# Kernel optimization log

Measured on AMD Instinct MI355X. Metric: run time of the kernel, lower is better.

The kernel has to match this reference:

```python
import jax, jax.numpy as jnp
import numpy as np

B, L, D, H = 2, 2048, 1024, 16
HD = D // H


def setup_inputs() -> dict:
    key = jax.random.key(0)
    ks = jax.random.split(key, 12)
    s = 1.0 / np.sqrt(D)
    inp = {
        "q": jax.random.normal(ks[0], (B, L, D), jnp.float32),
        "k": jax.random.normal(ks[1], (B, L, D), jnp.float32),
        "v": jax.random.normal(ks[2], (B, L, D), jnp.float32),
        "mask": jnp.zeros((B, L), dtype=bool),  # True = masked out
        "Wq": jax.random.normal(ks[3], (D, D), jnp.float32) * s,
        "bq": jnp.zeros((D,), jnp.float32),
        "Wk": jax.random.normal(ks[4], (D, D), jnp.float32) * s,
        "bk": jnp.zeros((D,), jnp.float32),
        "Wv": jax.random.normal(ks[5], (D, D), jnp.float32) * s,
        "bv": jnp.zeros((D,), jnp.float32),
        "Wo": jax.random.normal(ks[6], (D, D), jnp.float32) * s,
        "bo": jnp.zeros((D,), jnp.float32),
    }
    return inp


def reference(q, k, v, mask, Wq, bq, Wk, bk, Wv, bv, Wo, bo):
    # linear projections (torch Linear: x @ W.T + b), split into heads: [B,H,L,HD]
    def proj(x, W, b):
        y = jnp.einsum('bld,ed->ble', x, W) + b
        return y.reshape(x.shape[0], x.shape[1], H, HD).transpose(0, 2, 1, 3)

    Q = proj(q, Wq, bq)
    K = proj(k, Wk, bk)
    V = proj(v, Wv, bv)

    scale = 1.0 / np.sqrt(HD).astype(np.float32)
    scores = jnp.einsum('bhqd,bhkd->bhqk', Q, K) * scale  # [B,H,Lq,Lk]
    # mask [B,Lk] -> broadcast over heads and query positions
    scores = jnp.where(mask[:, None, None, :], -jnp.inf, scores)
    attn = jax.nn.softmax(scores, axis=-1)
    out = jnp.einsum('bhqk,bhkd->bhqd', attn, V)  # [B,H,Lq,HD]
    out = out.transpose(0, 2, 1, 3).reshape(q.shape[0], q.shape[1], D)
    return jnp.einsum('bld,ed->ble', out, Wo) + bo
```

## Files before the change

### kernel.cpp

```cpp
#include <hip/hip_runtime.h>

#define LSEQ 2048
#define DMODEL 1024
#define NHEAD 16
#define HDIM 64

typedef __attribute__((ext_vector_type(8))) short bf16x8;
typedef __attribute__((ext_vector_type(4))) float f32x4;
typedef __attribute__((ext_vector_type(16))) float f32x16;
typedef unsigned int u32;
typedef unsigned short u16;

static __device__ __forceinline__ u16 f2bf(float x) {
    return (u16)((__builtin_bit_cast(u32, x) + 0x8000u) >> 16);
}

static __device__ __forceinline__ u32 f2bf_pk(float hi, float lo) {
    u32 a = __builtin_bit_cast(u32, hi) + 0x8000u;
    u32 b = __builtin_bit_cast(u32, lo) + 0x8000u;
#if __has_builtin(__builtin_amdgcn_perm)
    return __builtin_amdgcn_perm(a, b, 0x07060302u);
#else
    return (a & 0xFFFF0000u) | (b >> 16);
#endif
}

static __device__ __forceinline__ float fast_exp2(float x) {
#if __has_builtin(__builtin_amdgcn_exp2f)
    return __builtin_amdgcn_exp2f(x);
#else
    return __expf(x * 0.6931471805599453f);
#endif
}

static __device__ __forceinline__ void gll16(const void* g, void* l) {
    __builtin_amdgcn_global_load_lds(
        (const __attribute__((address_space(1))) u32*)g,
        (__attribute__((address_space(3))) u32*)l, 16, 0, 0);
}

__global__ __launch_bounds__(256) void conv_all(
    const float* __restrict__ q, const float* __restrict__ k, const float* __restrict__ v,
    const float* __restrict__ w0, const float* __restrict__ w1,
    const float* __restrict__ w2, const float* __restrict__ w3,
    u16* __restrict__ Qf, u16* __restrict__ Kf, u16* __restrict__ Vf,
    u16* __restrict__ o0, u16* __restrict__ o1, u16* __restrict__ o2,
    u16* __restrict__ o3) {
    const int z = blockIdx.y;
    const float* s; u16* d;
    if (z == 0)      { s = q;  d = Qf; }
    else if (z == 1) { s = k;  d = Kf; }
    else if (z == 2) { s = v;  d = Vf; }
    else if (z == 3) { s = w0; d = o0; }
    else if (z == 4) { s = w1; d = o1; }
    else if (z == 5) { s = w2; d = o2; }
    else             { s = w3; d = o3; }
    if (z >= 3 && blockIdx.x >= 1024) return;
    const int i = (blockIdx.x * 256 + threadIdx.x) * 4;
    float4 x = *(const float4*)(s + i);
    uint2 r;
    r.x = f2bf_pk(x.y, x.x);
    r.y = f2bf_pk(x.w, x.z);
    *(uint2*)(d + i) = r;
}

template <int OUT_MODE>
__device__ __forceinline__ void mfma_gemm(const u16* __restrict__ Xb,
                                          const u16* __restrict__ Wb,
                                          const float* __restrict__ bias,
                                          void* __restrict__ Yv) {
    __shared__ alignas(16) u16 As[128 * 32];
    __shared__ alignas(16) u16 Bs[128 * 32];

    const int tid = threadIdx.x;
    const int wave = tid >> 6, lane = tid & 63;
    const int l16 = lane & 15, quad = lane >> 4;
    const int wm = (wave >> 1) * 64, wn = (wave & 1) * 64;
    const int m0 = blockIdx.x * 128, n0 = blockIdx.y * 128;

    f32x4 acc[4][4];
    #pragma unroll
    for (int i = 0; i < 4; ++i)
        #pragma unroll
        for (int j = 0; j < 4; ++j)
            #pragma unroll
            for (int r = 0; r < 4; ++r) acc[i][j][r] = 0.0f;

    for (int k0 = 0; k0 < DMODEL; k0 += 32) {
        __syncthreads();
        gll16(Xb + (size_t)(m0 + (tid >> 2)) * DMODEL + k0 + (tid & 3) * 8,
              As + tid * 8);
        gll16(Xb + (size_t)(m0 + 64 + (tid >> 2)) * DMODEL + k0 + (tid & 3) * 8,
              As + 2048 + tid * 8);
        gll16(Wb + (size_t)(n0 + (tid >> 2)) * DMODEL + k0 + (tid & 3) * 8,
              Bs + tid * 8);
        gll16(Wb + (size_t)(n0 + 64 + (tid >> 2)) * DMODEL + k0 + (tid & 3) * 8,
              Bs + 2048 + tid * 8);
        __syncthreads();

        bf16x8 af[4], bf[4];
        #pragma unroll
        for (int mb = 0; mb < 4; ++mb)
            af[mb] = *(const bf16x8*)(As + (wm + mb * 16 + l16) * 32 + quad * 8);
        #pragma unroll
        for (int nb = 0; nb < 4; ++nb)
            bf[nb] = *(const bf16x8*)(Bs + (wn + nb * 16 + l16) * 32 + quad * 8);
        #pragma unroll
        for (int mb = 0; mb < 4; ++mb)
            #pragma unroll
            for (int nb = 0; nb < 4; ++nb)
                acc[mb][nb] = __builtin_amdgcn_mfma_f32_16x16x32_bf16(
                    af[mb], bf[nb], acc[mb][nb], 0, 0, 0);
    }

    #pragma unroll
    for (int nb = 0; nb < 4; ++nb) {
        const int n = n0 + wn + nb * 16 + l16;
        const float bn = bias[n];
        #pragma unroll
        for (int mb = 0; mb < 4; ++mb) {
            const int mb0 = m0 + wm + mb * 16 + quad * 4;
            if (OUT_MODE == 2) {
                u16* Y = (u16*)Yv;
                uint2 rr;
                rr.x = f2bf_pk(acc[mb][nb][1] + bn, acc[mb][nb][0] + bn);
                rr.y = f2bf_pk(acc[mb][nb][3] + bn, acc[mb][nb][2] + bn);
                const int bb = mb0 >> 11, l = mb0 & 2047;
                const int h = n >> 6, hd = n & 63;
                *(uint2*)(Y + ((size_t)((bb * NHEAD + h) * HDIM) + hd) * LSEQ + l) = rr;
            } else {
                #pragma unroll
                for (int r = 0; r < 4; ++r) {
                    const int m = mb0 + r;
                    const float val = acc[mb][nb][r] + bn;
                    if (OUT_MODE == 0) {
                        u16* Y = (u16*)Yv;
                        const int bb = m >> 11, l = m & 2047;
                        const int h = n >> 6, hd = n & 63;
                        Y[(((size_t)(bb * NHEAD + h) * LSEQ + l) * HDIM) + hd] = f2bf(val);
                    } else {
                        float* Y = (float*)Yv;
                        Y[(size_t)m * DMODEL + n] = val;
                    }
                }
            }
        }
    }
}

__global__ __launch_bounds__(256) void qkv_gemm(
    const u16* __restrict__ Qf, const u16* __restrict__ Kf, const u16* __restrict__ Vf,
    const u16* __restrict__ Wqb, const u16* __restrict__ Wkb, const u16* __restrict__ Wvb,
    const float* __restrict__ bq, const float* __restrict__ bk, const float* __restrict__ bv,
    u16* __restrict__ Qp, u16* __restrict__ Kp, u16* __restrict__ Vtp) {
    if (blockIdx.z == 0)      mfma_gemm<0>(Qf, Wqb, bq, (void*)Qp);
    else if (blockIdx.z == 1) mfma_gemm<0>(Kf, Wkb, bk, (void*)Kp);
    else                      mfma_gemm<2>(Vf, Wvb, bv, (void*)Vtp);
}

__global__ __launch_bounds__(256) void out_gemm(
    const u16* __restrict__ AOb, const u16* __restrict__ Wob,
    const float* __restrict__ bo, float* __restrict__ out) {
    mfma_gemm<1>(AOb, Wob, bo, (void*)out);
}

#define KT 128

__global__ __launch_bounds__(256, 2) void attn_mfma(
    const u16* __restrict__ Qp, const u16* __restrict__ Kp,
    const u16* __restrict__ Vtp, const unsigned char* __restrict__ mask,
    u16* __restrict__ AOb) {
    __shared__ alignas(16) u16 smem[32768];

    const int tid = threadIdx.x;
    const int wave = tid >> 6;
    const int lane = tid & 63;
    const int l32 = lane & 31;
    const int half = lane >> 5;
    const int bh = blockIdx.x;
    const int b = bh >> 4;
    const int h = bh & 15;
    const int q0 = blockIdx.y * 128;
    const int qw = q0 + wave * 32;

    const u16* Qg = Qp + ((size_t)bh * LSEQ + qw) * HDIM;
    const u16* Kg = Kp + (size_t)bh * LSEQ * HDIM;
    const u16* Vtg = Vtp + (size_t)bh * HDIM * LSEQ;
    const unsigned char* mg = mask + (size_t)b * LSEQ;

    bf16x8 qf[4];
    #pragma unroll
    for (int dc = 0; dc < 4; ++dc)
        qf[dc] = *(const bf16x8*)(Qg + (size_t)l32 * HDIM + dc * 16 + half * 8);

    f32x16 o0 = {}, o1 = {};
    float m_l = -1e30f, l_l = 0.0f;
    const float SC = 0.125f * 1.4426950408889634f;

    auto stage = [&](int ktile, int buf) {
        const int k0 = ktile * KT;
        u16* Kb = smem + buf * 8192;
        u16* Vb = smem + 16384 + buf * 8192;
        #pragma unroll
        for (int j = 0; j < 4; ++j) {
            const int cid = j * 256 + tid;
            const int key = cid >> 3, pc = cid & 7, c = pc ^ (key & 7);
            gll16(Kg + (size_t)(k0 + key) * HDIM + c * 8, Kb + cid * 8);
        }
        #pragma unroll
        for (int j = 0; j < 4; ++j) {
            const int cid = j * 256 + tid;
            const int d = cid >> 4, pc = cid & 15, c = pc ^ (d & 15);
            gll16(Vtg + (size_t)d * LSEQ + k0 + c * 8, Vb + cid * 8);
        }
    };

    stage(0, 0);

    for (int kt = 0; kt < LSEQ / KT; ++kt) {
        const int cur = kt & 1;
        const u16* Kb = smem + cur * 8192;
        const u16* Vb = smem + 16384 + cur * 8192;
        const int k0 = kt * KT;
        const int mb0 = mg[k0 + lane];
        const int mb1 = mg[k0 + 64 + lane];

        __syncthreads();
        if (kt + 1 < LSEQ / KT) stage(kt + 1, cur ^ 1);

        f32x16 st[4];
        #pragma unroll
        for (int kb = 0; kb < 4; ++kb) st[kb] = (f32x16)(0.0f);
        #pragma unroll
        for (int dc = 0; dc < 4; ++dc)
            #pragma unroll
            for (int kb = 0; kb < 4; ++kb) {
                const int key = kb * 32 + l32;
                const int phys = (dc * 2 + half) ^ (key & 7);
                bf16x8 kf = *(const bf16x8*)(Kb + key * 64 + phys * 8);
                st[kb] = __builtin_amdgcn_mfma_f32_32x32x16_bf16(kf, qf[dc], st[kb], 0, 0, 0);
            }

        const unsigned long long anym = __ballot(mb0 | mb1);
        if (anym) {
            const float b0f = mb0 ? -1e30f : 0.0f;
            const float b1f = mb1 ? -1e30f : 0.0f;
            #pragma unroll
            for (int kb = 0; kb < 4; ++kb)
                #pragma unroll
                for (int r = 0; r < 16; ++r) {
                    const int key = kb * 32 + (r & 3) + 8 * (r >> 2) + 4 * half;
                    const float bv = __shfl((kb < 2) ? b0f : b1f, key & 63, 64);
                    st[kb][r] += bv;
                }
        }

        float mx = st[0][0];
        #pragma unroll
        for (int kb = 0; kb < 4; ++kb)
            #pragma unroll
            for (int r = 0; r < 16; ++r) mx = fmaxf(mx, st[kb][r]);
        mx = fmaxf(mx, __shfl_xor(mx, 32, 64));
        const float mnew = fmaxf(m_l, mx);
        const float msc = mnew * SC;
        const float alpha = fast_exp2(m_l * SC - msc);
        m_l = mnew;

        u32 pk[4][8];
        float rs = 0.0f;
        #pragma unroll
        for (int kb = 0; kb < 4; ++kb)
            #pragma unroll
            for (int w = 0; w < 8; ++w) {
                const float plo = fast_exp2(st[kb][2 * w] * SC - msc);
                const float phi = fast_exp2(st[kb][2 * w + 1] * SC - msc);
                rs += plo + phi;
                pk[kb][w] = f2bf_pk(phi, plo);
            }
        rs += __shfl_xor(rs, 32, 64);
        l_l = l_l * alpha + rs;
        #pragma unroll
        for (int r = 0; r < 16; ++r) { o0[r] *= alpha; o1[r] *= alpha; }

        #pragma unroll
        for (int c = 0; c < 8; ++c) {
            const int kb = c >> 1, wb = 4 * (c & 1);
            const u32 ta = half ? pk[kb][wb] : pk[kb][wb + 2];
            const u32 tb = half ? pk[kb][wb + 1] : pk[kb][wb + 3];
            const u32 xa = __shfl_xor((int)ta, 32, 64);
            const u32 xb = __shfl_xor((int)tb, 32, 64);
            u32 w4[4];
            w4[0] = half ? xa : pk[kb][wb];
            w4[1] = half ? xb : pk[kb][wb + 1];
            w4[2] = half ? pk[kb][wb + 2] : xa;
            w4[3] = half ? pk[kb][wb + 3] : xb;
            bf16x8 pb = __builtin_bit_cast(bf16x8, *(uint4*)w4);
            {
                const int d = l32;
                const int phys = (c * 2 + half) ^ (d & 15);
                bf16x8 va = *(const bf16x8*)(Vb + d * 128 + phys * 8);
                o0 = __builtin_amdgcn_mfma_f32_32x32x16_bf16(va, pb, o0, 0, 0, 0);
            }
            {
                const int d = 32 + l32;
                const int phys = (c * 2 + half) ^ (d & 15);
                bf16x8 va = *(const bf16x8*)(Vb + d * 128 + phys * 8);
                o1 = __builtin_amdgcn_mfma_f32_32x32x16_bf16(va, pb, o1, 0, 0, 0);
            }
        }
    }

    const float inv = 1.0f / l_l;
    __syncthreads();
    u16* T = smem;
    #pragma unroll
    for (int nb = 0; nb < 2; ++nb)
        #pragma unroll
        for (int rp = 0; rp < 8; ++rp) {
            const int r = rp * 2;
            const int d = nb * 32 + (r & 3) + 8 * (r >> 2) + 4 * half;
            const float vlo = (nb ? o1[r] : o0[r]) * inv;
            const float vhi = (nb ? o1[r + 1] : o0[r + 1]) * inv;
            *(u32*)(T + (wave * 32 + l32) * 72 + d) = f2bf_pk(vhi, vlo);
        }
    __syncthreads();
    #pragma unroll
    for (int i = 0; i < 4; ++i) {
        const int cid = i * 256 + tid;
        const int row = cid >> 3, ch = cid & 7;
        bf16x8 val = *(const bf16x8*)(T + row * 72 + ch * 8);
        *(bf16x8*)(AOb + ((size_t)(b * LSEQ + q0 + row) * DMODEL) + h * HDIM + ch * 8) = val;
    }
}

extern "C" void kernel_launch(void* const* d_in, const int* in_sizes, int n_in,
                              void* d_out, int out_size, void* d_ws, size_t ws_size,
                              hipStream_t stream) {
    (void)in_sizes; (void)n_in; (void)out_size; (void)ws_size;
    const float* q  = (const float*)d_in[0];
    const float* k  = (const float*)d_in[1];
    const float* v  = (const float*)d_in[2];
    const unsigned char* mask = (const unsigned char*)d_in[3];
    const float* Wq = (const float*)d_in[4];
    const float* bq = (const float*)d_in[5];
    const float* Wk = (const float*)d_in[6];
    const float* bk = (const float*)d_in[7];
    const float* Wv = (const float*)d_in[8];
    const float* bv = (const float*)d_in[9];
    const float* Wo = (const float*)d_in[10];
    const float* bo = (const float*)d_in[11];
    float* out = (float*)d_out;

    u16* ws16 = (u16*)d_ws;
    const size_t M4 = (size_t)4 * 1024 * 1024;
    const size_t M1 = (size_t)1024 * 1024;
    u16* Qf  = ws16;
    u16* Kf  = ws16 + M4;
    u16* Vf  = ws16 + 2 * M4;
    u16* Qp  = ws16 + 3 * M4;
    u16* Kp  = ws16 + 4 * M4;
    u16* Vtp = ws16 + 5 * M4;
    u16* AOb = ws16 + 6 * M4;
    u16* Wqb = ws16 + 7 * M4;
    u16* Wkb = ws16 + 7 * M4 + M1;
    u16* Wvb = ws16 + 7 * M4 + 2 * M1;
    u16* Wob = ws16 + 7 * M4 + 3 * M1;

    conv_all<<<dim3(4096, 7), 256, 0, stream>>>(q, k, v, Wq, Wk, Wv, Wo,
                                                Qf, Kf, Vf, Wqb, Wkb, Wvb, Wob);
    qkv_gemm<<<dim3(32, 8, 3), 256, 0, stream>>>(Qf, Kf, Vf, Wqb, Wkb, Wvb,
                                                 bq, bk, bv, Qp, Kp, Vtp);
    attn_mfma<<<dim3(32, 16), 256, 0, stream>>>(Qp, Kp, Vtp, mask, AOb);
    out_gemm<<<dim3(32, 8), 256, 0, stream>>>(AOb, Wob, bo, out);
}
```

Baseline: 240.6 us.

## Split attention over KV halves with combine kernel; widen GEMM K-tile with swizzle

Attention now splits the key sequence into two halves (grid z=2) and writes unnormalized bf16 partial outputs plus per-row max and sum. A new combine kernel merges the two halves. The aim is to double the block count from 512 and raise occupancy by using smaller KV tiles (64) and a higher launch bound. The GEMMs also move to a 64-wide K step with XOR-swizzled LDS layout, halving barrier count and avoiding bank conflicts. The cost is an extra kernel launch, extra partial-output traffic, and bf16 rounding of the unnormalized partials.

```diff
diff --git a/kernel.cpp b/kernel.cpp
--- a/kernel.cpp
+++ b/kernel.cpp
@@ -23,6 +23,10 @@
 #else
     return (a & 0xFFFF0000u) | (b >> 16);
 #endif
+}
+
+static __device__ __forceinline__ float bf2f(u16 x) {
+    return __builtin_bit_cast(float, (u32)x << 16);
 }
 
 static __device__ __forceinline__ float fast_exp2(float x) {
@@ -69,8 +73,8 @@
                                           const u16* __restrict__ Wb,
                                           const float* __restrict__ bias,
                                           void* __restrict__ Yv) {
-    __shared__ alignas(16) u16 As[128 * 32];
-    __shared__ alignas(16) u16 Bs[128 * 32];
+    __shared__ alignas(16) u16 As[128 * 64];
+    __shared__ alignas(16) u16 Bs[128 * 64];
 
     const int tid = threadIdx.x;
     const int wave = tid >> 6, lane = tid & 63;
@@ -86,31 +90,39 @@
             #pragma unroll
             for (int r = 0; r < 4; ++r) acc[i][j][r] = 0.0f;
 
-    for (int k0 = 0; k0 < DMODEL; k0 += 32) {
+    for (int k0 = 0; k0 < DMODEL; k0 += 64) {
         __syncthreads();
-        gll16(Xb + (size_t)(m0 + (tid >> 2)) * DMODEL + k0 + (tid & 3) * 8,
-              As + tid * 8);
-        gll16(Xb + (size_t)(m0 + 64 + (tid >> 2)) * DMODEL + k0 + (tid & 3) * 8,
-              As + 2048 + tid * 8);
-        gll16(Wb + (size_t)(n0 + (tid >> 2)) * DMODEL + k0 + (tid & 3) * 8,
-              Bs + tid * 8);
-        gll16(Wb + (size_t)(n0 + 64 + (tid >> 2)) * DMODEL + k0 + (tid & 3) * 8,
-              Bs + 2048 + tid * 8);
+        #pragma unroll
+        for (int j = 0; j < 4; ++j) {
+            const int cid = j * 256 + tid;
+            const int row = cid >> 3, pc = cid & 7, c = pc ^ (row & 7);
+            gll16(Xb + (size_t)(m0 + row) * DMODEL + k0 + c * 8, As + cid * 8);
+            gll16(Wb + (size_t)(n0 + row) * DMODEL + k0 + c * 8, Bs + cid * 8);
+        }
         __syncthreads();
 
-        bf16x8 af[4], bf[4];
-        #pragma unroll
-        for (int mb = 0; mb < 4; ++mb)
-            af[mb] = *(const bf16x8*)(As + (wm + mb * 16 + l16) * 32 + quad * 8);
-        #pragma unroll
-        for (int nb = 0; nb < 4; ++nb)
-            bf[nb] = *(const bf16x8*)(Bs + (wn + nb * 16 + l16) * 32 + quad * 8);
-        #pragma unroll
-        for (int mb = 0; mb < 4; ++mb)
-            #pragma unroll
-            for (int nb = 0; nb < 4; ++nb)
-                acc[mb][nb] = __builtin_amdgcn_mfma_f32_16x16x32_bf16(
-                    af[mb], bf[nb], acc[mb][nb], 0, 0, 0);
+        #pragma unroll
+        for (int c = 0; c < 2; ++c) {
+            bf16x8 af[4], bf[4];
+            #pragma unroll
+            for (int mb = 0; mb < 4; ++mb) {
+                const int row = wm + mb * 16 + l16;
+                const int phys = (c * 4 + quad) ^ (row & 7);
+                af[mb] = *(const bf16x8*)(As + row * 64 + phys * 8);
+            }
+            #pragma unroll
+            for (int nb = 0; nb < 4; ++nb) {
+                const int row = wn + nb * 16 + l16;
+                const int phys = (c * 4 + quad) ^ (row & 7);
+                bf[nb] = *(const bf16x8*)(Bs + row * 64 + phys * 8);
+            }
+            #pragma unroll
+            for (int mb = 0; mb < 4; ++mb)
+                #pragma unroll
+                for (int nb = 0; nb < 4; ++nb)
+                    acc[mb][nb] = __builtin_amdgcn_mfma_f32_16x16x32_bf16(
+                        af[mb], bf[nb], acc[mb][nb], 0, 0, 0);
+        }
     }
 
     #pragma unroll
@@ -164,13 +176,13 @@
     mfma_gemm<1>(AOb, Wob, bo, (void*)out);
 }
 
-#define KT 128
-
-__global__ __launch_bounds__(256, 2) void attn_mfma(
+#define KT 64
+
+__global__ __launch_bounds__(256, 4) void attn_mfma(
     const u16* __restrict__ Qp, const u16* __restrict__ Kp,
     const u16* __restrict__ Vtp, const unsigned char* __restrict__ mask,
-    u16* __restrict__ AOb) {
-    __shared__ alignas(16) u16 smem[32768];
+    u16* __restrict__ Opart, float* __restrict__ mp, float* __restrict__ lp) {
+    __shared__ alignas(16) u16 smem[16384];
 
     const int tid = threadIdx.x;
     const int wave = tid >> 6;
@@ -179,14 +191,14 @@
     const int half = lane >> 5;
     const int bh = blockIdx.x;
     const int b = bh >> 4;
-    const int h = bh & 15;
     const int q0 = blockIdx.y * 128;
+    const int split = blockIdx.z;
     const int qw = q0 + wave * 32;
 
     const u16* Qg = Qp + ((size_t)bh * LSEQ + qw) * HDIM;
-    const u16* Kg = Kp + (size_t)bh * LSEQ * HDIM;
-    const u16* Vtg = Vtp + (size_t)bh * HDIM * LSEQ;
-    const unsigned char* mg = mask + (size_t)b * LSEQ;
+    const u16* Kg = Kp + ((size_t)bh * LSEQ + split * 1024) * HDIM;
+    const u16* Vtg = Vtp + (size_t)bh * HDIM * LSEQ + split * 1024;
+    const unsigned char* mg = mask + (size_t)b * LSEQ + split * 1024;
 
     bf16x8 qf[4];
     #pragma unroll
@@ -197,67 +209,64 @@
     float m_l = -1e30f, l_l = 0.0f;
     const float SC = 0.125f * 1.4426950408889634f;
 
-    auto stage = [&](int ktile, int buf) {
-        const int k0 = ktile * KT;
-        u16* Kb = smem + buf * 8192;
-        u16* Vb = smem + 16384 + buf * 8192;
-        #pragma unroll
-        for (int j = 0; j < 4; ++j) {
+    auto stage = [&](int kt_, int buf) {
+        const int k0 = kt_ * KT;
+        u16* Kb = smem + buf * 4096;
+        u16* Vb = smem + 8192 + buf * 4096;
+        #pragma unroll
+        for (int j = 0; j < 2; ++j) {
             const int cid = j * 256 + tid;
             const int key = cid >> 3, pc = cid & 7, c = pc ^ (key & 7);
             gll16(Kg + (size_t)(k0 + key) * HDIM + c * 8, Kb + cid * 8);
         }
         #pragma unroll
-        for (int j = 0; j < 4; ++j) {
+        for (int j = 0; j < 2; ++j) {
             const int cid = j * 256 + tid;
-            const int d = cid >> 4, pc = cid & 15, c = pc ^ (d & 15);
+            const int d = cid >> 3, pc = cid & 7, c = pc ^ (d & 7);
             gll16(Vtg + (size_t)d * LSEQ + k0 + c * 8, Vb + cid * 8);
         }
     };
 
     stage(0, 0);
 
-    for (int kt = 0; kt < LSEQ / KT; ++kt) {
+    for (int kt = 0; kt < 1024 / KT; ++kt) {
         const int cur = kt & 1;
-        const u16* Kb = smem + cur * 8192;
-        const u16* Vb = smem + 16384 + cur * 8192;
+        const u16* Kb = smem + cur * 4096;
+        const u16* Vb = smem + 8192 + cur * 4096;
         const int k0 = kt * KT;
-        const int mb0 = mg[k0 + lane];
-        const int mb1 = mg[k0 + 64 + lane];
+        const int mb = mg[k0 + lane];
 
         __syncthreads();
-        if (kt + 1 < LSEQ / KT) stage(kt + 1, cur ^ 1);
-
-        f32x16 st[4];
-        #pragma unroll
-        for (int kb = 0; kb < 4; ++kb) st[kb] = (f32x16)(0.0f);
+        if (kt + 1 < 1024 / KT) stage(kt + 1, cur ^ 1);
+
+        f32x16 st[2];
+        st[0] = (f32x16)(0.0f);
+        st[1] = (f32x16)(0.0f);
         #pragma unroll
         for (int dc = 0; dc < 4; ++dc)
             #pragma unroll
-            for (int kb = 0; kb < 4; ++kb) {
+            for (int kb = 0; kb < 2; ++kb) {
                 const int key = kb * 32 + l32;
                 const int phys = (dc * 2 + half) ^ (key & 7);
                 bf16x8 kf = *(const bf16x8*)(Kb + key * 64 + phys * 8);
                 st[kb] = __builtin_amdgcn_mfma_f32_32x32x16_bf16(kf, qf[dc], st[kb], 0, 0, 0);
             }
 
-        const unsigned long long anym = __ballot(mb0 | mb1);
+        const unsigned long long anym = __ballot(mb);
         if (anym) {
-            const float b0f = mb0 ? -1e30f : 0.0f;
-            const float b1f = mb1 ? -1e30f : 0.0f;
-            #pragma unroll
-            for (int kb = 0; kb < 4; ++kb)
+            const float bf = mb ? -1e30f : 0.0f;
+            #pragma unroll
+            for (int kb = 0; kb < 2; ++kb)
                 #pragma unroll
                 for (int r = 0; r < 16; ++r) {
                     const int key = kb * 32 + (r & 3) + 8 * (r >> 2) + 4 * half;
-                    const float bv = __shfl((kb < 2) ? b0f : b1f, key & 63, 64);
-                    st[kb][r] += bv;
+                    st[kb][r] += __shfl(bf, key, 64);
                 }
         }
 
         float mx = st[0][0];
         #pragma unroll
-        for (int kb = 0; kb < 4; ++kb)
+        for (int kb = 0; kb < 2; ++kb)
             #pragma unroll
             for (int r = 0; r < 16; ++r) mx = fmaxf(mx, st[kb][r]);
         mx = fmaxf(mx, __shfl_xor(mx, 32, 64));
@@ -266,10 +275,10 @@
         const float alpha = fast_exp2(m_l * SC - msc);
         m_l = mnew;
 
-        u32 pk[4][8];
+        u32 pk[2][8];
         float rs = 0.0f;
         #pragma unroll
-        for (int kb = 0; kb < 4; ++kb)
+        for (int kb = 0; kb < 2; ++kb)
             #pragma unroll
             for (int w = 0; w < 8; ++w) {
                 const float plo = fast_exp2(st[kb][2 * w] * SC - msc);
@@ -283,7 +292,7 @@
         for (int r = 0; r < 16; ++r) { o0[r] *= alpha; o1[r] *= alpha; }
 
         #pragma unroll
-        for (int c = 0; c < 8; ++c) {
+        for (int c = 0; c < 4; ++c) {
             const int kb = c >> 1, wb = 4 * (c & 1);
             const u32 ta = half ? pk[kb][wb] : pk[kb][wb + 2];
             const u32 tb = half ? pk[kb][wb + 1] : pk[kb][wb + 3];
@@ -297,20 +306,25 @@
             bf16x8 pb = __builtin_bit_cast(bf16x8, *(uint4*)w4);
             {
                 const int d = l32;
-                const int phys = (c * 2 + half) ^ (d & 15);
-                bf16x8 va = *(const bf16x8*)(Vb + d * 128 + phys * 8);
+                const int phys = (c * 2 + half) ^ (d & 7);
+                bf16x8 va = *(const bf16x8*)(Vb + d * 64 + phys * 8);
                 o0 = __builtin_amdgcn_mfma_f32_32x32x16_bf16(va, pb, o0, 0, 0, 0);
             }
             {
                 const int d = 32 + l32;
-                const int phys = (c * 2 + half) ^ (d & 15);
-                bf16x8 va = *(const bf16x8*)(Vb + d * 128 + phys * 8);
+                const int phys = (c * 2 + half) ^ (d & 7);
+                bf16x8 va = *(const bf16x8*)(Vb + d * 64 + phys * 8);
                 o1 = __builtin_amdgcn_mfma_f32_32x32x16_bf16(va, pb, o1, 0, 0, 0);
             }
         }
     }
 
-    const float inv = 1.0f / l_l;
+    if (half == 0) {
+        const size_t idx = ((size_t)split * 32 + bh) * LSEQ + qw + l32;
+        mp[idx] = m_l;
+        lp[idx] = l_l;
+    }
+
     __syncthreads();
     u16* T = smem;
     #pragma unroll
@@ -319,8 +333,8 @@
         for (int rp = 0; rp < 8; ++rp) {
             const int r = rp * 2;
             const int d = nb * 32 + (r & 3) + 8 * (r >> 2) + 4 * half;
-            const float vlo = (nb ? o1[r] : o0[r]) * inv;
-            const float vhi = (nb ? o1[r + 1] : o0[r + 1]) * inv;
+            const float vlo = nb ? o1[r] : o0[r];
+            const float vhi = nb ? o1[r + 1] : o0[r + 1];
             *(u32*)(T + (wave * 32 + l32) * 72 + d) = f2bf_pk(vhi, vlo);
         }
     __syncthreads();
@@ -329,7 +343,40 @@
         const int cid = i * 256 + tid;
         const int row = cid >> 3, ch = cid & 7;
         bf16x8 val = *(const bf16x8*)(T + row * 72 + ch * 8);
-        *(bf16x8*)(AOb + ((size_t)(b * LSEQ + q0 + row) * DMODEL) + h * HDIM + ch * 8) = val;
+        *(bf16x8*)(Opart + (((size_t)split * 32 + bh) * LSEQ + q0 + row) * HDIM + ch * 8) = val;
+    }
+}
+
+__global__ __launch_bounds__(256) void attn_combine(
+    const u16* __restrict__ Opart, const float* __restrict__ mp,
+    const float* __restrict__ lp, u16* __restrict__ AOb) {
+    const int q = blockIdx.x * 256 + threadIdx.x;
+    const int bh = blockIdx.y, b = bh >> 4, h = bh & 15;
+    const size_t i0 = (size_t)bh * LSEQ + q;
+    const size_t i1 = (size_t)32 * LSEQ + i0;
+    const float m0 = mp[i0], m1 = mp[i1];
+    const float l0 = lp[i0], l1 = lp[i1];
+    const float SC = 0.125f * 1.4426950408889634f;
+    const float mm = fmaxf(m0, m1);
+    float a0 = fast_exp2((m0 - mm) * SC);
+    float a1 = fast_exp2((m1 - mm) * SC);
+    const float inv = 1.0f / (l0 * a0 + l1 * a1);
+    a0 *= inv; a1 *= inv;
+    const u16* p0 = Opart + i0 * HDIM;
+    const u16* p1 = Opart + i1 * HDIM;
+    u16* dst = AOb + ((size_t)b * LSEQ + q) * DMODEL + h * HDIM;
+    #pragma unroll
+    for (int c = 0; c < 8; ++c) {
+        bf16x8 x0 = *(const bf16x8*)(p0 + c * 8);
+        bf16x8 x1 = *(const bf16x8*)(p1 + c * 8);
+        union { bf16x8 v; u16 u[8]; } r;
+        #pragma unroll
+        for (int j = 0; j < 8; ++j) {
+            const float f0 = bf2f((u16)x0[j]);
+            const float f1 = bf2f((u16)x1[j]);
+            r.u[j] = f2bf(f0 * a0 + f1 * a1);
+        }
+        *(bf16x8*)(dst + c * 8) = r.v;
     }
 }
 
@@ -357,6 +404,9 @@
     u16* Qf  = ws16;
     u16* Kf  = ws16 + M4;
     u16* Vf  = ws16 + 2 * M4;
+    u16* Opart = ws16;
+    float* mpf = (float*)(ws16 + 2 * M4);
+    float* lpf = mpf + 2 * 32 * LSEQ;
     u16* Qp  = ws16 + 3 * M4;
     u16* Kp  = ws16 + 4 * M4;
     u16* Vtp = ws16 + 5 * M4;
@@ -370,6 +420,8 @@
                                                 Qf, Kf, Vf, Wqb, Wkb, Wvb, Wob);
     qkv_gemm<<<dim3(32, 8, 3), 256, 0, stream>>>(Qf, Kf, Vf, Wqb, Wkb, Wvb,
                                                  bq, bk, bv, Qp, Kp, Vtp);
-    attn_mfma<<<dim3(32, 16), 256, 0, stream>>>(Qp, Kp, Vtp, mask, AOb);
+    attn_mfma<<<dim3(32, 16, 2), 256, 0, stream>>>(Qp, Kp, Vtp, mask,
+                                                   Opart, mpf, lpf);
+    attn_combine<<<dim3(LSEQ / 256, 32), 256, 0, stream>>>(Opart, mpf, lpf, AOb);
     out_gemm<<<dim3(32, 8), 256, 0, stream>>>(AOb, Wob, bo, out);
 }
```

New measurement: 269.0 us. 1.12x slower.
